# Performance work log

Hardware: AMD Instinct MI355X
Metric: run time of the kernel (lower is better)

Reference implementation:

```python
import jax, jax.numpy as jnp
import numpy as np

NUM_HEADS = 16
HEAD_DIM = 64


def setup_inputs() -> dict:
    key = jax.random.key(0)
    k1, k2, k3 = jax.random.split(key, 3)
    B, S, D = 2, 2048, 1024
    scale = 1.0 / np.sqrt(D)
    return {
        "x": jax.random.normal(k1, (B, S, D), dtype=jnp.float32),
        "W_qkv": jax.random.normal(k2, (D, 3 * D), dtype=jnp.float32) * scale,
        "b_qkv": jnp.zeros((3 * D,), dtype=jnp.float32),
        "W_o": jax.random.normal(k3, (D, D), dtype=jnp.float32) * scale,
        "b_o": jnp.zeros((D,), dtype=jnp.float32),
    }


def reference(x, W_qkv, b_qkv, W_o, b_o):
    B, S, D = x.shape
    H, Hd = NUM_HEADS, HEAD_DIM
    qkv = x @ W_qkv + b_qkv                      # [B, S, 3D]
    qkv = qkv.reshape(B, S, H, 3 * Hd).transpose(0, 2, 1, 3)  # [B, H, S, 3Hd]
    q, k, v = jnp.split(qkv, 3, axis=-1)         # each [B, H, S, Hd]
    # negative squared Euclidean distance: -(|q|^2 - 2 q.k + |k|^2)
    q_sq = jnp.sum(q * q, axis=-1)[..., :, None]   # [B, H, S, 1]
    k_sq = jnp.sum(k * k, axis=-1)[..., None, :]   # [B, H, 1, S]
    qk = jnp.einsum("bhsd,bhtd->bhst", q, k)       # [B, H, S, S]
    logits = -(q_sq - 2.0 * qk + k_sq)
    attn = jax.nn.softmax(logits, axis=-1)
    vals = jnp.einsum("bhst,bhtd->bhsd", attn, v)  # [B, H, S, Hd]
    vals = vals.transpose(0, 2, 1, 3).reshape(B, S, D)
    return vals @ W_o + b_o
```

## Files before the change

kernel.cpp:

```cpp
#include <hip/hip_runtime.h>
#include <hip/hip_bf16.h>

#define NUM_B   2
#define SEQ     2048
#define DMODEL  1024
#define NH      16
#define HD      64
#define M_TOT   (NUM_B * SEQ)
#define N_QKV   (3 * DMODEL)
#define LOG2E   1.4426950408889634f
#define EXP_BIAS 96.0f

typedef __attribute__((ext_vector_type(8))) short short8v;
typedef __attribute__((ext_vector_type(4))) float float4v;
typedef unsigned short ushort_t;

__device__ __forceinline__ ushort_t f2bf(float x) {
    unsigned u = __builtin_bit_cast(unsigned, x);
    u = u + 0x7FFFu + ((u >> 16) & 1u);
    return (ushort_t)(u >> 16);
}
__device__ __forceinline__ float bf2f(ushort_t h) {
    unsigned u = ((unsigned)h) << 16;
    return __builtin_bit_cast(float, u);
}
__device__ __forceinline__ void gll16(const void* g, void* l) {
    __builtin_amdgcn_global_load_lds(
        (const __attribute__((address_space(1))) unsigned int*)g,
        (__attribute__((address_space(3))) unsigned int*)l, 16, 0, 0);
}
__device__ __forceinline__ int sw4(int r) { return (r & 3) ^ ((r >> 2) & 3); }

__global__ __launch_bounds__(256) void prep_kernel(
    const float* __restrict__ Wq, const float* __restrict__ Wo,
    const float* __restrict__ Xf,
    ushort_t* __restrict__ WqT_hi, ushort_t* __restrict__ WqT_lo,
    ushort_t* __restrict__ WoT,
    ushort_t* __restrict__ Xhi, ushort_t* __restrict__ Xlo)
{
    const int bid = blockIdx.x;
    const int t = threadIdx.x;

    if (bid >= 1024) {
        size_t base = (size_t)(bid - 1024) * 4096 + t * 16;
        float xs[16];
        *(float4v*)&xs[0]  = *(const float4v*)(Xf + base);
        *(float4v*)&xs[4]  = *(const float4v*)(Xf + base + 4);
        *(float4v*)&xs[8]  = *(const float4v*)(Xf + base + 8);
        *(float4v*)&xs[12] = *(const float4v*)(Xf + base + 12);
        short8v h0, h1, l0, l1;
        #pragma unroll
        for (int e = 0; e < 8; e++) {
            ushort_t a = f2bf(xs[e]), b = f2bf(xs[8 + e]);
            h0[e] = (short)a; h1[e] = (short)b;
            l0[e] = (short)f2bf(xs[e] - bf2f(a));
            l1[e] = (short)f2bf(xs[8 + e] - bf2f(b));
        }
        *(short8v*)(Xhi + base) = h0; *(short8v*)(Xhi + base + 8) = h1;
        *(short8v*)(Xlo + base) = l0; *(short8v*)(Xlo + base + 8) = l1;
        return;
    }

    __shared__ float Tf[64][65];
    const float* src; ushort_t *dhi, *dlo; int N, k0, n0;
    if (bid < 768) {
        int kt = bid / 48, nt = bid % 48;
        src = Wq; N = N_QKV; dhi = WqT_hi; dlo = WqT_lo;
        k0 = kt * 64; n0 = nt * 64;
    } else {
        int tid = bid - 768;
        int kt = tid >> 4, nt = tid & 15;
        src = Wo; N = DMODEL; dhi = WoT; dlo = nullptr;
        k0 = kt * 64; n0 = nt * 64;
    }
    {
        int r = t >> 2, c0 = (t & 3) * 16;
        const float* srow = src + (size_t)(k0 + r) * N + n0 + c0;
        #pragma unroll
        for (int u = 0; u < 4; u++) {
            float4v f = *(const float4v*)(srow + 4 * u);
            #pragma unroll
            for (int e = 0; e < 4; e++) Tf[r][c0 + 4 * u + e] = f[e];
        }
    }
    __syncthreads();
    {
        int nl = t >> 2, kc = (t & 3) * 16;
        short8v h0, h1, l0, l1;
        #pragma unroll
        for (int e = 0; e < 8; e++) {
            float x0 = Tf[kc + e][nl];
            float x1 = Tf[kc + 8 + e][nl];
            ushort_t a = f2bf(x0), b = f2bf(x1);
            h0[e] = (short)a; h1[e] = (short)b;
            l0[e] = (short)f2bf(x0 - bf2f(a));
            l1[e] = (short)f2bf(x1 - bf2f(b));
        }
        ushort_t* o = dhi + (size_t)(n0 + nl) * 1024 + k0 + kc;
        *(short8v*)o = h0; *(short8v*)(o + 8) = h1;
        if (dlo) {
            ushort_t* o2 = dlo + (size_t)(n0 + nl) * 1024 + k0 + kc;
            *(short8v*)o2 = l0; *(short8v*)(o2 + 8) = l1;
        }
    }
}

__global__ __launch_bounds__(512, 2) void qkv_mfma256_kernel(
    const ushort_t* __restrict__ Xhi, const ushort_t* __restrict__ Xlo,
    const ushort_t* __restrict__ WqT_hi, const ushort_t* __restrict__ WqT_lo,
    const float* __restrict__ bias,
    ushort_t* __restrict__ Qhi, ushort_t* __restrict__ Qlo,
    ushort_t* __restrict__ Khi, ushort_t* __restrict__ Klo,
    ushort_t* __restrict__ Vout,
    float* __restrict__ Qsq, float* __restrict__ Ksq)
{
    __shared__ ushort_t AS [2 * 2 * 8192];
    __shared__ ushort_t BSh[2 * 2 * 8192];
    const int SLAB = 8192;
    const int BUFS = 2 * SLAB;

    const int t    = threadIdx.x;
    const int w    = t >> 6;
    const int quad = (t >> 4) & 3, ln = t & 15;
    const int wr = w >> 2, wc = w & 3;
    const int bx = blockIdx.x, by = blockIdx.y;
    const int p  = bx >> 2, bq = bx & 3;
    const int m0 = by * 256;
    const bool qk = (p != 2);
    const int h  = 4 * bq + wc;
    const int g  = p + 3 * h;

    const ushort_t* gA[2]; const ushort_t* gB[2]; int lOff[2];
    #pragma unroll
    for (int i = 0; i < 2; i++) {
        int c = 512 * i + t;
        int r = c >> 2, kb = c & 3;
        gA[i] = Xhi + (size_t)(m0 + r) * 1024 + 8 * (kb ^ sw4(r));
        int hj = 4 * bq + (r >> 6);
        int ng = 192 * hj + 64 * p + (r & 63);
        gB[i] = WqT_hi + (size_t)ng * 1024 + 8 * (kb ^ sw4(r));
        lOff[i] = (512 * i + 64 * w) * 8;
    }
    const size_t xlo_off = (size_t)(Xlo - Xhi);
    const size_t wlo_off = (size_t)(WqT_lo - WqT_hi);

    int aoff[8], boff[4];
    #pragma unroll
    for (int mt = 0; mt < 8; mt++) {
        int m_l = 128 * wr + 16 * mt + ln;
        aoff[mt] = m_l * 32 + ((quad ^ sw4(m_l)) << 3);
    }
    #pragma unroll
    for (int nt = 0; nt < 4; nt++) {
        int n_l = 64 * wc + 16 * nt + ln;
        boff[nt] = n_l * 32 + ((quad ^ sw4(n_l)) << 3);
    }

    float4v acc[8][4];
    #pragma unroll
    for (int i = 0; i < 8; i++)
        #pragma unroll
        for (int j = 0; j < 4; j++) acc[i][j] = (float4v){0.f, 0.f, 0.f, 0.f};

    auto stage = [&](int ks, int buf) {
        const int kk = 32 * ks;
        ushort_t* Ab = &AS [buf * BUFS];
        ushort_t* Bb = &BSh[buf * BUFS];
        #pragma unroll
        for (int i = 0; i < 2; i++) {
            gll16(gA[i] + kk, Ab + lOff[i]);
            gll16(gB[i] + kk, Bb + lOff[i]);
        }
        if (qk) {
            #pragma unroll
            for (int i = 0; i < 2; i++) {
                gll16(gA[i] + kk + xlo_off, Ab + SLAB + lOff[i]);
                gll16(gB[i] + kk + wlo_off, Bb + SLAB + lOff[i]);
            }
        }
    };

    const int NKS = DMODEL / 32;
    stage(0, 0);
    __syncthreads();

    for (int ks = 0; ks < NKS; ks++) {
        const int buf = ks & 1;
        if (ks + 1 < NKS) stage(ks + 1, buf ^ 1);

        const ushort_t* Ab = &AS [buf * BUFS];
        const ushort_t* Bb = &BSh[buf * BUFS];

        short8v bh4[4], bl4[4];
        #pragma unroll
        for (int nt = 0; nt < 4; nt++) {
            bh4[nt] = *(const short8v*)(Bb + boff[nt]);
            if (qk) bl4[nt] = *(const short8v*)(Bb + SLAB + boff[nt]);
        }
        #pragma unroll
        for (int mt = 0; mt < 8; mt++) {
            short8v ahm = *(const short8v*)(Ab + aoff[mt]);
            if (qk) {
                short8v alm = *(const short8v*)(Ab + SLAB + aoff[mt]);
                #pragma unroll
                for (int nt = 0; nt < 4; nt++) {
                    acc[mt][nt] = __builtin_amdgcn_mfma_f32_16x16x32_bf16(ahm, bh4[nt], acc[mt][nt], 0, 0, 0);
                    acc[mt][nt] = __builtin_amdgcn_mfma_f32_16x16x32_bf16(ahm, bl4[nt], acc[mt][nt], 0, 0, 0);
                    acc[mt][nt] = __builtin_amdgcn_mfma_f32_16x16x32_bf16(alm, bh4[nt], acc[mt][nt], 0, 0, 0);
                }
            } else {
                #pragma unroll
                for (int nt = 0; nt < 4; nt++)
                    acc[mt][nt] = __builtin_amdgcn_mfma_f32_16x16x32_bf16(ahm, bh4[nt], acc[mt][nt], 0, 0, 0);
            }
        }
        __syncthreads();
    }

    float bvv[4];
    #pragma unroll
    for (int nt = 0; nt < 4; nt++) bvv[nt] = bias[64 * g + 16 * nt + ln];

    #pragma unroll
    for (int mt = 0; mt < 8; mt++) {
        #pragma unroll
        for (int r = 0; r < 4; r++) {
            int m = m0 + 128 * wr + 16 * mt + 4 * quad + r;
            int bb = m >> 11, s = m & (SEQ - 1);
            size_t hsrow = (size_t)(bb * NH + h) * SEQ + s;
            size_t rowbase = hsrow * HD;
            float vv[4];
            #pragma unroll
            for (int nt = 0; nt < 4; nt++) vv[nt] = acc[mt][nt][r] + bvv[nt];
            if (p == 0) {
                float sq = 0.f;
                #pragma unroll
                for (int nt = 0; nt < 4; nt++) {
                    float v = vv[nt];
                    sq += v * v;
                    float v2 = v * (2.0f * LOG2E);
                    ushort_t hb = f2bf(v2);
                    Qhi[rowbase + 16 * nt + ln] = hb;
                    Qlo[rowbase + 16 * nt + ln] = f2bf(v2 - bf2f(hb));
                }
                sq += __shfl_xor(sq, 1); sq += __shfl_xor(sq, 2);
                sq += __shfl_xor(sq, 4); sq += __shfl_xor(sq, 8);
                if (ln == 0) Qsq[hsrow] = sq * LOG2E - EXP_BIAS;
            } else if (p == 1) {
                float sq = 0.f;
                #pragma unroll
                for (int nt = 0; nt < 4; nt++) {
                    float v = vv[nt];
                    sq += v * v;
                    ushort_t hb = f2bf(v);
                    Khi[rowbase + 16 * nt + ln] = hb;
                    Klo[rowbase + 16 * nt + ln] = f2bf(v - bf2f(hb));
                }
                sq += __shfl_xor(sq, 1); sq += __shfl_xor(sq, 2);
                sq += __shfl_xor(sq, 4); sq += __shfl_xor(sq, 8);
                if (ln == 0) Ksq[hsrow] = sq * LOG2E;
            } else {
                #pragma unroll
                for (int nt = 0; nt < 4; nt++)
                    Vout[((size_t)(bb * NH + h) * 64 + 16 * nt + ln) * SEQ + s] = f2bf(vv[nt]);
            }
        }
    }
}

template<bool PRE>
__global__ __launch_bounds__(256) void qkv_mfma_kernel(
    const float* __restrict__ X,
    const ushort_t* __restrict__ Xhi, const ushort_t* __restrict__ Xlo,
    const ushort_t* __restrict__ WqT_hi, const ushort_t* __restrict__ WqT_lo,
    const float* __restrict__ bias,
    ushort_t* __restrict__ Qhi, ushort_t* __restrict__ Qlo,
    ushort_t* __restrict__ Khi, ushort_t* __restrict__ Klo,
    ushort_t* __restrict__ Vout,
    float* __restrict__ Qsq, float* __restrict__ Ksq)
{
    __shared__ ushort_t AS2[2 * 128 * 32];
    __shared__ ushort_t BS [2 * 128 * 32];
    const int LO = 128 * 32;
    const int t = threadIdx.x;
    const int w = t >> 6, lane = t & 63;
    const int quad = (t >> 4) & 3, ln = t & 15;
    const int wr = w >> 1, wc = w & 1;
    const int m0 = blockIdx.y * 128, n0 = blockIdx.x * 128;
    const int g = blockIdx.x * 2 + wc;
    const int h = g / 3, part = g % 3;

    const ushort_t* gA[2]; ushort_t* lA[2];
    const float* aptr = nullptr;
    ushort_t *ast_hi0, *ast_hi1, *ast_lo0, *ast_lo1;
    size_t xlo_off = 0;
    if constexpr (PRE) {
        #pragma unroll
        for (int i = 0; i < 2; i++) {
            int c = 256 * i + 64 * w + lane;
            int r = c >> 2, kbp = c & 3;
            gA[i] = Xhi + (size_t)(m0 + r) * 1024 + 8 * (kbp ^ sw4(r));
            lA[i] = &AS2[(256 * i + 64 * w) * 8];
        }
        xlo_off = (size_t)(Xlo - Xhi);
    } else {
        const int arow = t >> 1, akh = t & 1;
        aptr = X + (size_t)(m0 + arow) * DMODEL + 16 * akh;
        const int asw = sw4(arow);
        ast_hi0 = &AS2[arow * 32 + (((2 * akh) ^ asw) << 3)];
        ast_hi1 = &AS2[arow * 32 + (((2 * akh + 1) ^ asw) << 3)];
        ast_lo0 = &AS2[LO + arow * 32 + (((2 * akh) ^ asw) << 3)];
        ast_lo1 = &AS2[LO + arow * 32 + (((2 * akh + 1) ^ asw) << 3)];
    }

    const ushort_t* gB[2]; ushort_t* lB[2];
    #pragma unroll
    for (int i = 0; i < 2; i++) {
        int c = 256 * i + 64 * w + lane;
        int n = c >> 2, kbp = c & 3;
        gB[i] = WqT_hi + (size_t)(n0 + n) * 1024 + 8 * (kbp ^ sw4(n));
        lB[i] = &BS[(256 * i + 64 * w) * 8];
    }
    const size_t lo_goff = (size_t)(WqT_lo - WqT_hi);

    int aoff[4], boff[4];
    #pragma unroll
    for (int i = 0; i < 4; i++) {
        int m_l = 64 * wr + 16 * i + ln;
        aoff[i] = m_l * 32 + ((quad ^ sw4(m_l)) << 3);
        int n_l = 64 * wc + 16 * i + ln;
        boff[i] = n_l * 32 + ((quad ^ sw4(n_l)) << 3);
    }

    float4v acc[4][4];
    #pragma unroll
    for (int i = 0; i < 4; i++)
        #pragma unroll
        for (int j = 0; j < 4; j++) acc[i][j] = (float4v){0.f, 0.f, 0.f, 0.f};

    for (int k0 = 0; k0 < DMODEL; k0 += 32) {
        __syncthreads();
        #pragma unroll
        for (int i = 0; i < 2; i++) {
            gll16(gB[i] + k0, lB[i]);
            gll16(gB[i] + k0 + lo_goff, lB[i] + LO);
        }
        if constexpr (PRE) {
            #pragma unroll
            for (int i = 0; i < 2; i++) {
                gll16(gA[i] + k0, lA[i]);
                gll16(gA[i] + k0 + xlo_off, lA[i] + LO);
            }
        } else {
            float xs[16];
            *(float4v*)&xs[0]  = *(const float4v*)(aptr + k0);
            *(float4v*)&xs[4]  = *(const float4v*)(aptr + k0 + 4);
            *(float4v*)&xs[8]  = *(const float4v*)(aptr + k0 + 8);
            *(float4v*)&xs[12] = *(const float4v*)(aptr + k0 + 12);
            short8v h0, h1, l0, l1;
            #pragma unroll
            for (int e = 0; e < 8; e++) {
                ushort_t a = f2bf(xs[e]), b = f2bf(xs[8 + e]);
                h0[e] = (short)a; h1[e] = (short)b;
                l0[e] = (short)f2bf(xs[e] - bf2f(a));
                l1[e] = (short)f2bf(xs[8 + e] - bf2f(b));
            }
            *(short8v*)ast_hi0 = h0; *(short8v*)ast_hi1 = h1;
            *(short8v*)ast_lo0 = l0; *(short8v*)ast_lo1 = l1;
        }
        __syncthreads();

        short8v ah[4], al[4], bh[4], bl[4];
        #pragma unroll
        for (int i = 0; i < 4; i++) {
            ah[i] = *(short8v*)&AS2[aoff[i]];
            al[i] = *(short8v*)&AS2[LO + aoff[i]];
            bh[i] = *(short8v*)&BS[boff[i]];
            bl[i] = *(short8v*)&BS[LO + boff[i]];
        }
        if (part != 2) {
            #pragma unroll
            for (int mt = 0; mt < 4; mt++)
                #pragma unroll
                for (int nt = 0; nt < 4; nt++) {
                    acc[mt][nt] = __builtin_amdgcn_mfma_f32_16x16x32_bf16(ah[mt], bh[nt], acc[mt][nt], 0, 0, 0);
                    acc[mt][nt] = __builtin_amdgcn_mfma_f32_16x16x32_bf16(ah[mt], bl[nt], acc[mt][nt], 0, 0, 0);
                    acc[mt][nt] = __builtin_amdgcn_mfma_f32_16x16x32_bf16(al[mt], bh[nt], acc[mt][nt], 0, 0, 0);
                }
        } else {
            #pragma unroll
            for (int mt = 0; mt < 4; mt++)
                #pragma unroll
                for (int nt = 0; nt < 4; nt++)
                    acc[mt][nt] = __builtin_amdgcn_mfma_f32_16x16x32_bf16(ah[mt], bh[nt], acc[mt][nt], 0, 0, 0);
        }
    }

    float bvv[4];
    #pragma unroll
    for (int nt = 0; nt < 4; nt++) bvv[nt] = bias[64 * g + 16 * nt + ln];

    #pragma unroll
    for (int mt = 0; mt < 4; mt++) {
        #pragma unroll
        for (int r = 0; r < 4; r++) {
            int m = m0 + 64 * wr + 16 * mt + 4 * quad + r;
            int bb = m >> 11, s = m & (SEQ - 1);
            size_t hsrow = (size_t)(bb * NH + h) * SEQ + s;
            size_t rowbase = hsrow * HD;
            float vv[4];
            #pragma unroll
            for (int nt = 0; nt < 4; nt++) vv[nt] = acc[mt][nt][r] + bvv[nt];
            if (part == 0) {
                float sq = 0.f;
                #pragma unroll
                for (int nt = 0; nt < 4; nt++) {
                    float v = vv[nt];
                    sq += v * v;
                    float v2 = v * (2.0f * LOG2E);
                    ushort_t hb = f2bf(v2);
                    Qhi[rowbase + 16 * nt + ln] = hb;
                    Qlo[rowbase + 16 * nt + ln] = f2bf(v2 - bf2f(hb));
                }
                sq += __shfl_xor(sq, 1); sq += __shfl_xor(sq, 2);
                sq += __shfl_xor(sq, 4); sq += __shfl_xor(sq, 8);
                if (ln == 0) Qsq[hsrow] = sq * LOG2E - EXP_BIAS;
            } else if (part == 1) {
                float sq = 0.f;
                #pragma unroll
                for (int nt = 0; nt < 4; nt++) {
                    float v = vv[nt];
                    sq += v * v;
                    ushort_t hb = f2bf(v);
                    Khi[rowbase + 16 * nt + ln] = hb;
                    Klo[rowbase + 16 * nt + ln] = f2bf(v - bf2f(hb));
                }
                sq += __shfl_xor(sq, 1); sq += __shfl_xor(sq, 2);
                sq += __shfl_xor(sq, 4); sq += __shfl_xor(sq, 8);
                if (ln == 0) Ksq[hsrow] = sq * LOG2E;
            } else {
                #pragma unroll
                for (int nt = 0; nt < 4; nt++)
                    Vout[rowbase + 16 * nt + ln] = f2bf(vv[nt]);
            }
        }
    }
}

template<bool PRE>
__global__ __launch_bounds__(256, 4) void attn_mfma_kernel(
    const ushort_t* __restrict__ Qhi, const ushort_t* __restrict__ Qlo,
    const ushort_t* __restrict__ Khi, const ushort_t* __restrict__ Klo,
    const ushort_t* __restrict__ Vsrc,
    const float* __restrict__ Qsq, const float* __restrict__ Ksq,
    ushort_t* __restrict__ vals)
{
    __shared__ ushort_t KS[2 * 64 * 64];
    __shared__ ushort_t VtS [64 * 64];
    __shared__ ushort_t PsS [64 * 72];
    const int LO = 64 * 64;

    const int t    = threadIdx.x;
    const int w    = t >> 6, lane = t & 63;
    const int quad = (t >> 4) & 3, ln = t & 15;
    const int bh   = blockIdx.y;
    const int q0   = blockIdx.x * 64;
    const size_t base  = (size_t)bh * SEQ * HD;
    const size_t baseS = (size_t)bh * SEQ;

    short8v qhi[2], qlo[2];
    float4v qsq4;
    {
        size_t ro = base + (size_t)(q0 + 16 * w + ln) * HD + quad * 8;
        qhi[0] = *(const short8v*)(Qhi + ro);
        qhi[1] = *(const short8v*)(Qhi + ro + 32);
        qlo[0] = *(const short8v*)(Qlo + ro);
        qlo[1] = *(const short8v*)(Qlo + ro + 32);
        qsq4 = *(const float4v*)(Qsq + baseS + q0 + 16 * w + 4 * quad);
    }

    const ushort_t* gK[2]; ushort_t* lK[2];
    #pragma unroll
    for (int i = 0; i < 2; i++) {
        int c = 256 * i + 64 * w + lane;
        int key = c >> 3, dbp = c & 7;
        gK[i] = Khi + base + (size_t)key * HD + 8 * (dbp ^ (key & 7));
        lK[i] = &KS[(256 * i + 64 * w) * 8];
    }
    const size_t kloff = (size_t)(Klo - Khi);

    const ushort_t* gV[2]; ushort_t* lV[2];
    if constexpr (PRE) {
        #pragma unroll
        for (int i = 0; i < 2; i++) {
            int c = 256 * i + 64 * w + lane;
            int d = c >> 3, kc = c & 7;
            gV[i] = Vsrc + ((size_t)bh * 64 + d) * SEQ + 8 * (kc ^ (d & 7));
            lV[i] = &VtS[(256 * i + 64 * w) * 8];
        }
    }

    float4v accO[4];
    float lsum[4];
    #pragma unroll
    for (int nt = 0; nt < 4; nt++) accO[nt] = (float4v){0.f, 0.f, 0.f, 0.f};
    #pragma unroll
    for (int r = 0; r < 4; r++) lsum[r] = 0.f;

    for (int kt = 0; kt < SEQ; kt += 64) {
        __syncthreads();
        #pragma unroll
        for (int i = 0; i < 2; i++) {
            gll16(gK[i] + (size_t)kt * HD, lK[i]);
            gll16(gK[i] + (size_t)kt * HD + kloff, lK[i] + LO);
        }
        if constexpr (PRE) {
            #pragma unroll
            for (int i = 0; i < 2; i++)
                gll16(gV[i] + kt, lV[i]);
        } else {
            #pragma unroll
            for (int i = 0; i < 2; i++) {
                int c = t + 256 * i;
                int key = c >> 3, db = c & 7;
                short8v v8 = *(const short8v*)(Vsrc + base + (size_t)(kt + key) * HD + 8 * db);
                #pragma unroll
                for (int e = 0; e < 8; e++) {
                    int col = key ^ (e << 3);
                    VtS[(8 * db + e) * 64 + col] = (ushort_t)v8[e];
                }
            }
        }
        float ksq_c[4];
        #pragma unroll
        for (int nt = 0; nt < 4; nt++)
            ksq_c[nt] = Ksq[baseS + kt + 16 * nt + ln];
        __syncthreads();

        float4v accS[4];
        #pragma unroll
        for (int nt = 0; nt < 4; nt++) accS[nt] = (float4v){0.f, 0.f, 0.f, 0.f};

        #pragma unroll
        for (int nt = 0; nt < 4; nt++) {
            int keyrow = 16 * nt + ln;
            #pragma unroll
            for (int c = 0; c < 2; c++) {
                int db  = quad + 4 * c;
                int off = keyrow * 64 + ((db ^ (keyrow & 7)) << 3);
                short8v bh_ = *(short8v*)&KS[off];
                short8v bl_ = *(short8v*)&KS[LO + off];
                accS[nt] = __builtin_amdgcn_mfma_f32_16x16x32_bf16(qhi[c], bh_, accS[nt], 0, 0, 0);
                accS[nt] = __builtin_amdgcn_mfma_f32_16x16x32_bf16(qhi[c], bl_, accS[nt], 0, 0, 0);
                accS[nt] = __builtin_amdgcn_mfma_f32_16x16x32_bf16(qlo[c], bh_, accS[nt], 0, 0, 0);
            }
        }

        #pragma unroll
        for (int nt = 0; nt < 4; nt++) {
            float pv[4];
            #pragma unroll
            for (int r = 0; r < 4; r++) {
                float p = exp2f(accS[nt][r] - ksq_c[nt] - qsq4[r]);
                lsum[r] += p;
                pv[r] = p;
            }
            unsigned int pk01, pk23;
            asm("v_cvt_pk_bf16_f32 %0, %1, %2" : "=v"(pk01) : "v"(pv[0]), "v"(pv[1]));
            asm("v_cvt_pk_bf16_f32 %0, %1, %2" : "=v"(pk23) : "v"(pv[2]), "v"(pv[3]));
            ushort_t* pp = &PsS[(16 * w + 4 * quad) * 72 + 16 * nt + ln];
            pp[0]       = (ushort_t)(pk01 & 0xffffu);
            pp[72]      = (ushort_t)(pk01 >> 16);
            pp[144]     = (ushort_t)(pk23 & 0xffffu);
            pp[216]     = (ushort_t)(pk23 >> 16);
        }
        __syncthreads();

        #pragma unroll
        for (int c = 0; c < 2; c++) {
            short8v aP = *(short8v*)&PsS[(16 * w + ln) * 72 + quad * 8 + 32 * c];
            #pragma unroll
            for (int nt = 0; nt < 4; nt++) {
                int drow = 16 * nt + ln;
                int db   = quad + 4 * c;
                int off  = drow * 64 + ((db ^ (drow & 7)) << 3);
                short8v bV = *(short8v*)&VtS[off];
                accO[nt] = __builtin_amdgcn_mfma_f32_16x16x32_bf16(aP, bV, accO[nt], 0, 0, 0);
            }
        }
    }

    const int bb = bh >> 4, h = bh & 15;
    float inv[4];
    #pragma unroll
    for (int r = 0; r < 4; r++) {
        float s = lsum[r];
        s += __shfl_xor(s, 1); s += __shfl_xor(s, 2);
        s += __shfl_xor(s, 4); s += __shfl_xor(s, 8);
        inv[r] = 1.f / s;
    }
    #pragma unroll
    for (int nt = 0; nt < 4; nt++)
        #pragma unroll
        for (int r = 0; r < 4; r++) {
            int row = q0 + 16 * w + 4 * quad + r;
            vals[(size_t)(bb * SEQ + row) * DMODEL + h * 64 + 16 * nt + ln] =
                f2bf(accO[nt][r] * inv[r]);
        }
}

__global__ __launch_bounds__(256) void out_mfma_kernel(
    const ushort_t* __restrict__ Ab, const ushort_t* __restrict__ BT,
    const float* __restrict__ bias, float* __restrict__ out)
{
    __shared__ ushort_t AS[2 * 128 * 32], BSo[2 * 128 * 32];
    const int BUF = 128 * 32;
    const int t = threadIdx.x;
    const int w = t >> 6;
    const int quad = (t >> 4) & 3, ln = t & 15;
    const int wr = (w >> 1), wc = w & 1;
    const int m0 = blockIdx.y * 128, n0 = blockIdx.x * 128;

    const ushort_t* gA[2]; const ushort_t* gB[2]; int lOff[2];
    #pragma unroll
    for (int i = 0; i < 2; i++) {
        int c = 256 * i + t;
        int r = c >> 2, kbp = c & 3;
        gA[i] = Ab + (size_t)(m0 + r) * 1024 + 8 * (kbp ^ sw4(r));
        gB[i] = BT + (size_t)(n0 + r) * 1024 + 8 * (kbp ^ sw4(r));
        lOff[i] = (256 * i + 64 * w) * 8;
    }
    int aoff[4], boff[4];
    #pragma unroll
    for (int i = 0; i < 4; i++) {
        int m_l = 64 * wr + 16 * i + ln;
        aoff[i] = m_l * 32 + ((quad ^ sw4(m_l)) << 3);
        int n_l = 64 * wc + 16 * i + ln;
        boff[i] = n_l * 32 + ((quad ^ sw4(n_l)) << 3);
    }

    float4v acc[4][4];
    #pragma unroll
    for (int i = 0; i < 4; i++)
        #pragma unroll
        for (int j = 0; j < 4; j++) acc[i][j] = (float4v){0.f, 0.f, 0.f, 0.f};

    auto stage = [&](int ks, int buf) {
        const int kk = 32 * ks;
        #pragma unroll
        for (int i = 0; i < 2; i++) {
            gll16(gA[i] + kk, &AS [buf * BUF] + lOff[i]);
            gll16(gB[i] + kk, &BSo[buf * BUF] + lOff[i]);
        }
    };

    const int NKS = DMODEL / 32;
    stage(0, 0);
    __syncthreads();

    for (int ks = 0; ks < NKS; ks++) {
        const int buf = ks & 1;
        if (ks + 1 < NKS) stage(ks + 1, buf ^ 1);

        const ushort_t* Abuf = &AS [buf * BUF];
        const ushort_t* Bbuf = &BSo[buf * BUF];
        short8v a[4], b[4];
        #pragma unroll
        for (int i = 0; i < 4; i++) {
            a[i] = *(const short8v*)(Abuf + aoff[i]);
            b[i] = *(const short8v*)(Bbuf + boff[i]);
        }
        #pragma unroll
        for (int mt = 0; mt < 4; mt++)
            #pragma unroll
            for (int nt = 0; nt < 4; nt++)
                acc[mt][nt] = __builtin_amdgcn_mfma_f32_16x16x32_bf16(a[mt], b[nt], acc[mt][nt], 0, 0, 0);

        __syncthreads();
    }

    #pragma unroll
    for (int nt = 0; nt < 4; nt++) {
        int n = n0 + 64 * wc + 16 * nt + ln;
        float bv = bias[n];
        #pragma unroll
        for (int mt = 0; mt < 4; mt++)
            #pragma unroll
            for (int r = 0; r < 4; r++) {
                int m = m0 + 64 * wr + 16 * mt + 4 * quad + r;
                out[(size_t)m * DMODEL + n] = acc[mt][nt][r] + bv;
            }
    }
}

extern "C" void kernel_launch(void* const* d_in, const int* in_sizes, int n_in,
                              void* d_out, int out_size, void* d_ws, size_t ws_size,
                              hipStream_t stream) {
    const float* x     = (const float*)d_in[0];
    const float* W_qkv = (const float*)d_in[1];
    const float* b_qkv = (const float*)d_in[2];
    const float* W_o   = (const float*)d_in[3];
    const float* b_o   = (const float*)d_in[4];
    float* out = (float*)d_out;

    const size_t WQT = (size_t)N_QKV * DMODEL;
    const size_t WO  = (size_t)DMODEL * DMODEL;
    const size_t QE  = (size_t)NUM_B * NH * SEQ * HD;
    const size_t SQN = (size_t)NUM_B * NH * SEQ;

    const size_t NEED = (2 * WQT + WO + 5 * QE + 2 * QE) * 2 + 2 * SQN * 4;
    const bool pre = (ws_size >= NEED);

    ushort_t* ws     = (ushort_t*)d_ws;
    ushort_t* WqT_hi = ws;
    ushort_t* WqT_lo = WqT_hi + WQT;
    ushort_t* WoT    = WqT_lo + WQT;
    ushort_t* Qhi    = WoT + WO;
    ushort_t* Qlo    = Qhi + QE;
    ushort_t* Khi    = Qlo + QE;
    ushort_t* Klo    = Khi + QE;
    ushort_t* Vx     = Klo + QE;
    float*    Qsq; float* Ksq;
    ushort_t* valsb; ushort_t* Xhi = nullptr; ushort_t* Xlo = nullptr;

    if (pre) {
        Qsq   = (float*)(Vx + QE);
        Ksq   = Qsq + SQN;
        Xhi   = (ushort_t*)(Ksq + SQN);
        Xlo   = Xhi + QE;
        valsb = WqT_hi;
    } else {
        valsb = Vx + QE;
        Qsq   = (float*)(valsb + QE);
        Ksq   = Qsq + SQN;
    }

    prep_kernel<<<pre ? 2048 : 1024, 256, 0, stream>>>(
        W_qkv, W_o, x, WqT_hi, WqT_lo, WoT, Xhi, Xlo);
    if (pre) {
        qkv_mfma256_kernel<<<dim3(12, M_TOT / 256), 512, 0, stream>>>(
            Xhi, Xlo, WqT_hi, WqT_lo, b_qkv, Qhi, Qlo, Khi, Klo, Vx, Qsq, Ksq);
        attn_mfma_kernel<true><<<dim3(SEQ / 64, NUM_B * NH), 256, 0, stream>>>(
            Qhi, Qlo, Khi, Klo, Vx, Qsq, Ksq, valsb);
    } else {
        qkv_mfma_kernel<false><<<dim3(N_QKV / 128, M_TOT / 128), 256, 0, stream>>>(
            x, nullptr, nullptr, WqT_hi, WqT_lo, b_qkv, Qhi, Qlo, Khi, Klo, Vx, Qsq, Ksq);
        attn_mfma_kernel<false><<<dim3(SEQ / 64, NUM_B * NH), 256, 0, stream>>>(
            Qhi, Qlo, Khi, Klo, Vx, Qsq, Ksq, valsb);
    }
    out_mfma_kernel<<<dim3(DMODEL / 128, M_TOT / 128), 256, 0, stream>>>(
        valsb, WoT, b_o, out);
}
```

Before: 303.0 us.

## Unify QKV GEMM per head so each block computes Q, K, V together

```diff
diff --git a/kernel.cpp b/kernel.cpp
--- a/kernel.cpp
+++ b/kernel.cpp
@@ -14,6 +14,12 @@
 typedef __attribute__((ext_vector_type(8))) short short8v;
 typedef __attribute__((ext_vector_type(4))) float float4v;
 typedef unsigned short ushort_t;
+
+#if __has_builtin(__builtin_amdgcn_exp2f)
+#define EXP2F(x) __builtin_amdgcn_exp2f(x)
+#else
+#define EXP2F(x) exp2f(x)
+#endif
 
 __device__ __forceinline__ ushort_t f2bf(float x) {
     unsigned u = __builtin_bit_cast(unsigned, x);
@@ -105,7 +111,7 @@
     }
 }
 
-__global__ __launch_bounds__(512, 2) void qkv_mfma256_kernel(
+__global__ __launch_bounds__(512, 2) void qkv_uni_kernel(
     const ushort_t* __restrict__ Xhi, const ushort_t* __restrict__ Xlo,
     const ushort_t* __restrict__ WqT_hi, const ushort_t* __restrict__ WqT_lo,
     const float* __restrict__ bias,
@@ -114,70 +120,73 @@
     ushort_t* __restrict__ Vout,
     float* __restrict__ Qsq, float* __restrict__ Ksq)
 {
-    __shared__ ushort_t AS [2 * 2 * 8192];
-    __shared__ ushort_t BSh[2 * 2 * 8192];
-    const int SLAB = 8192;
-    const int BUFS = 2 * SLAB;
+    const int SLAB_A = 8192, BUFA = 16384;
+    const int SLAB_B = 6144, BUFB = 12288;
+    __shared__ ushort_t AS[2 * BUFA];
+    __shared__ ushort_t BS[2 * BUFB];
 
     const int t    = threadIdx.x;
     const int w    = t >> 6;
     const int quad = (t >> 4) & 3, ln = t & 15;
     const int wr = w >> 2, wc = w & 3;
-    const int bx = blockIdx.x, by = blockIdx.y;
-    const int p  = bx >> 2, bq = bx & 3;
-    const int m0 = by * 256;
-    const bool qk = (p != 2);
-    const int h  = 4 * bq + wc;
-    const int g  = p + 3 * h;
-
-    const ushort_t* gA[2]; const ushort_t* gB[2]; int lOff[2];
+    const int h  = blockIdx.x;
+    const int m0 = blockIdx.y * 256;
+
+    const ushort_t* gA[2]; int lOffA[2];
     #pragma unroll
     for (int i = 0; i < 2; i++) {
         int c = 512 * i + t;
         int r = c >> 2, kb = c & 3;
         gA[i] = Xhi + (size_t)(m0 + r) * 1024 + 8 * (kb ^ sw4(r));
-        int hj = 4 * bq + (r >> 6);
-        int ng = 192 * hj + 64 * p + (r & 63);
-        gB[i] = WqT_hi + (size_t)ng * 1024 + 8 * (kb ^ sw4(r));
-        lOff[i] = (512 * i + 64 * w) * 8;
+        lOffA[i] = (512 * i + 64 * w) * 8;
     }
     const size_t xlo_off = (size_t)(Xlo - Xhi);
-    const size_t wlo_off = (size_t)(WqT_lo - WqT_hi);
-
-    int aoff[8], boff[4];
+
+    const ushort_t* gBp[3]; int lOffB[3];
+    #pragma unroll
+    for (int i = 0; i < 3; i++) {
+        int c = 512 * i + t;
+        bool hi = c < 768;
+        int cc = hi ? c : c - 768;
+        int j = cc >> 2, kb = cc & 3;
+        int jj = j >> 4, jl = j & 15;
+        int wcq = jj / 3, part = jj % 3;
+        int ng = 192 * h + 64 * part + 16 * wcq + jl;
+        gBp[i] = (hi ? WqT_hi : WqT_lo) + (size_t)ng * 1024 + 8 * (kb ^ sw4(j));
+        int cwb = (512 * i + 64 * w) - (hi ? 0 : 768);
+        lOffB[i] = (hi ? 0 : SLAB_B) + cwb * 8;
+    }
+
+    int aoff[8], boff[3];
     #pragma unroll
     for (int mt = 0; mt < 8; mt++) {
         int m_l = 128 * wr + 16 * mt + ln;
         aoff[mt] = m_l * 32 + ((quad ^ sw4(m_l)) << 3);
     }
     #pragma unroll
-    for (int nt = 0; nt < 4; nt++) {
-        int n_l = 64 * wc + 16 * nt + ln;
-        boff[nt] = n_l * 32 + ((quad ^ sw4(n_l)) << 3);
-    }
-
-    float4v acc[8][4];
+    for (int p = 0; p < 3; p++) {
+        int j = 48 * wc + 16 * p + ln;
+        boff[p] = j * 32 + ((quad ^ sw4(j)) << 3);
+    }
+
+    float4v acc[8][3];
     #pragma unroll
     for (int i = 0; i < 8; i++)
         #pragma unroll
-        for (int j = 0; j < 4; j++) acc[i][j] = (float4v){0.f, 0.f, 0.f, 0.f};
+        for (int j = 0; j < 3; j++) acc[i][j] = (float4v){0.f, 0.f, 0.f, 0.f};
 
     auto stage = [&](int ks, int buf) {
         const int kk = 32 * ks;
-        ushort_t* Ab = &AS [buf * BUFS];
-        ushort_t* Bb = &BSh[buf * BUFS];
+        ushort_t* Ab = &AS[buf * BUFA];
+        ushort_t* Bb = &BS[buf * BUFB];
         #pragma unroll
         for (int i = 0; i < 2; i++) {
-            gll16(gA[i] + kk, Ab + lOff[i]);
-            gll16(gB[i] + kk, Bb + lOff[i]);
-        }
-        if (qk) {
-            #pragma unroll
-            for (int i = 0; i < 2; i++) {
-                gll16(gA[i] + kk + xlo_off, Ab + SLAB + lOff[i]);
-                gll16(gB[i] + kk + wlo_off, Bb + SLAB + lOff[i]);
-            }
-        }
+            gll16(gA[i] + kk, Ab + lOffA[i]);
+            gll16(gA[i] + kk + xlo_off, Ab + SLAB_A + lOffA[i]);
+        }
+        #pragma unroll
+        for (int i = 0; i < 3; i++)
+            gll16(gBp[i] + kk, Bb + lOffB[i]);
     };
 
     const int NKS = DMODEL / 32;
@@ -188,38 +197,35 @@
         const int buf = ks & 1;
         if (ks + 1 < NKS) stage(ks + 1, buf ^ 1);
 
-        const ushort_t* Ab = &AS [buf * BUFS];
-        const ushort_t* Bb = &BSh[buf * BUFS];
-
-        short8v bh4[4], bl4[4];
-        #pragma unroll
-        for (int nt = 0; nt < 4; nt++) {
-            bh4[nt] = *(const short8v*)(Bb + boff[nt]);
-            if (qk) bl4[nt] = *(const short8v*)(Bb + SLAB + boff[nt]);
-        }
+        const ushort_t* Ab = &AS[buf * BUFA];
+        const ushort_t* Bb = &BS[buf * BUFB];
+
+        short8v bh0 = *(const short8v*)(Bb + boff[0]);
+        short8v bh1 = *(const short8v*)(Bb + boff[1]);
+        short8v bh2 = *(const short8v*)(Bb + boff[2]);
+        short8v bl0 = *(const short8v*)(Bb + SLAB_B + boff[0]);
+        short8v bl1 = *(const short8v*)(Bb + SLAB_B + boff[1]);
+
         #pragma unroll
         for (int mt = 0; mt < 8; mt++) {
-            short8v ahm = *(const short8v*)(Ab + aoff[mt]);
-            if (qk) {
-                short8v alm = *(const short8v*)(Ab + SLAB + aoff[mt]);
-                #pragma unroll
-                for (int nt = 0; nt < 4; nt++) {
-                    acc[mt][nt] = __builtin_amdgcn_mfma_f32_16x16x32_bf16(ahm, bh4[nt], acc[mt][nt], 0, 0, 0);
-                    acc[mt][nt] = __builtin_amdgcn_mfma_f32_16x16x32_bf16(ahm, bl4[nt], acc[mt][nt], 0, 0, 0);
-                    acc[mt][nt] = __builtin_amdgcn_mfma_f32_16x16x32_bf16(alm, bh4[nt], acc[mt][nt], 0, 0, 0);
-                }
-            } else {
-                #pragma unroll
-                for (int nt = 0; nt < 4; nt++)
-                    acc[mt][nt] = __builtin_amdgcn_mfma_f32_16x16x32_bf16(ahm, bh4[nt], acc[mt][nt], 0, 0, 0);
-            }
+            short8v aH = *(const short8v*)(Ab + aoff[mt]);
+            short8v aL = *(const short8v*)(Ab + SLAB_A + aoff[mt]);
+            acc[mt][0] = __builtin_amdgcn_mfma_f32_16x16x32_bf16(aH, bh0, acc[mt][0], 0, 0, 0);
+            acc[mt][0] = __builtin_amdgcn_mfma_f32_16x16x32_bf16(aH, bl0, acc[mt][0], 0, 0, 0);
+            acc[mt][0] = __builtin_amdgcn_mfma_f32_16x16x32_bf16(aL, bh0, acc[mt][0], 0, 0, 0);
+            acc[mt][1] = __builtin_amdgcn_mfma_f32_16x16x32_bf16(aH, bh1, acc[mt][1], 0, 0, 0);
+            acc[mt][1] = __builtin_amdgcn_mfma_f32_16x16x32_bf16(aH, bl1, acc[mt][1], 0, 0, 0);
+            acc[mt][1] = __builtin_amdgcn_mfma_f32_16x16x32_bf16(aL, bh1, acc[mt][1], 0, 0, 0);
+            acc[mt][2] = __builtin_amdgcn_mfma_f32_16x16x32_bf16(aH, bh2, acc[mt][2], 0, 0, 0);
         }
         __syncthreads();
     }
 
-    float bvv[4];
-    #pragma unroll
-    for (int nt = 0; nt < 4; nt++) bvv[nt] = bias[64 * g + 16 * nt + ln];
+    const float bQ = bias[192 * h + 16 * wc + ln];
+    const float bK = bias[192 * h + 64 + 16 * wc + ln];
+    const float bV = bias[192 * h + 128 + 16 * wc + ln];
+    const int d = 16 * wc + ln;
+    float* sqbuf = (float*)AS;
 
     #pragma unroll
     for (int mt = 0; mt < 8; mt++) {
@@ -229,42 +235,48 @@
             int bb = m >> 11, s = m & (SEQ - 1);
             size_t hsrow = (size_t)(bb * NH + h) * SEQ + s;
             size_t rowbase = hsrow * HD;
-            float vv[4];
-            #pragma unroll
-            for (int nt = 0; nt < 4; nt++) vv[nt] = acc[mt][nt][r] + bvv[nt];
-            if (p == 0) {
-                float sq = 0.f;
-                #pragma unroll
-                for (int nt = 0; nt < 4; nt++) {
-                    float v = vv[nt];
-                    sq += v * v;
-                    float v2 = v * (2.0f * LOG2E);
-                    ushort_t hb = f2bf(v2);
-                    Qhi[rowbase + 16 * nt + ln] = hb;
-                    Qlo[rowbase + 16 * nt + ln] = f2bf(v2 - bf2f(hb));
-                }
-                sq += __shfl_xor(sq, 1); sq += __shfl_xor(sq, 2);
-                sq += __shfl_xor(sq, 4); sq += __shfl_xor(sq, 8);
-                if (ln == 0) Qsq[hsrow] = sq * LOG2E - EXP_BIAS;
-            } else if (p == 1) {
-                float sq = 0.f;
-                #pragma unroll
-                for (int nt = 0; nt < 4; nt++) {
-                    float v = vv[nt];
-                    sq += v * v;
-                    ushort_t hb = f2bf(v);
-                    Khi[rowbase + 16 * nt + ln] = hb;
-                    Klo[rowbase + 16 * nt + ln] = f2bf(v - bf2f(hb));
-                }
-                sq += __shfl_xor(sq, 1); sq += __shfl_xor(sq, 2);
-                sq += __shfl_xor(sq, 4); sq += __shfl_xor(sq, 8);
-                if (ln == 0) Ksq[hsrow] = sq * LOG2E;
-            } else {
-                #pragma unroll
-                for (int nt = 0; nt < 4; nt++)
-                    Vout[((size_t)(bb * NH + h) * 64 + 16 * nt + ln) * SEQ + s] = f2bf(vv[nt]);
-            }
-        }
+
+            float vQ = acc[mt][0][r] + bQ;
+            float vK = acc[mt][1][r] + bK;
+            float vV = acc[mt][2][r] + bV;
+
+            float v2 = vQ * (2.0f * LOG2E);
+            ushort_t hbq = f2bf(v2);
+            Qhi[rowbase + d] = hbq;
+            Qlo[rowbase + d] = f2bf(v2 - bf2f(hbq));
+            float sqq = vQ * vQ;
+            sqq += __shfl_xor(sqq, 1); sqq += __shfl_xor(sqq, 2);
+            sqq += __shfl_xor(sqq, 4); sqq += __shfl_xor(sqq, 8);
+
+            ushort_t hbk = f2bf(vK);
+            Khi[rowbase + d] = hbk;
+            Klo[rowbase + d] = f2bf(vK - bf2f(hbk));
+            float sqk = vK * vK;
+            sqk += __shfl_xor(sqk, 1); sqk += __shfl_xor(sqk, 2);
+            sqk += __shfl_xor(sqk, 4); sqk += __shfl_xor(sqk, 8);
+
+            Vout[((size_t)(bb * NH + h) * 64 + d) * SEQ + s] = f2bf(vV);
+
+            if (ln == 0) {
+                int rloc = 16 * mt + 4 * quad + r;
+                sqbuf[((0 * 2 + wr) * 4 + wc) * 128 + rloc] = sqq;
+                sqbuf[((1 * 2 + wr) * 4 + wc) * 128 + rloc] = sqk;
+            }
+        }
+    }
+    __syncthreads();
+    {
+        int sel = t >> 8, rid = t & 255;
+        int wrr = rid >> 7, rloc = rid & 127;
+        float s4 = sqbuf[((sel * 2 + wrr) * 4 + 0) * 128 + rloc]
+                 + sqbuf[((sel * 2 + wrr) * 4 + 1) * 128 + rloc]
+                 + sqbuf[((sel * 2 + wrr) * 4 + 2) * 128 + rloc]
+                 + sqbuf[((sel * 2 + wrr) * 4 + 3) * 128 + rloc];
+        int m = m0 + 128 * wrr + rloc;
+        int bb = m >> 11, s = m & (SEQ - 1);
+        size_t hsrow = (size_t)(bb * NH + h) * SEQ + s;
+        if (sel == 0) Qsq[hsrow] = s4 * LOG2E - EXP_BIAS;
+        else          Ksq[hsrow] = s4 * LOG2E;
     }
 }
 
@@ -469,14 +481,16 @@
     const size_t baseS = (size_t)bh * SEQ;
 
     short8v qhi[2], qlo[2];
-    float4v qsq4;
+    float nqsq4[4];
     {
         size_t ro = base + (size_t)(q0 + 16 * w + ln) * HD + quad * 8;
         qhi[0] = *(const short8v*)(Qhi + ro);
         qhi[1] = *(const short8v*)(Qhi + ro + 32);
         qlo[0] = *(const short8v*)(Qlo + ro);
         qlo[1] = *(const short8v*)(Qlo + ro + 32);
-        qsq4 = *(const float4v*)(Qsq + baseS + q0 + 16 * w + 4 * quad);
+        float4v q4 = *(const float4v*)(Qsq + baseS + q0 + 16 * w + 4 * quad);
+        #pragma unroll
+        for (int r = 0; r < 4; r++) nqsq4[r] = -q4[r];
     }
 
     const ushort_t* gK[2]; ushort_t* lK[2];
@@ -531,15 +545,17 @@
                 }
             }
         }
-        float ksq_c[4];
+        float nksq[4];
         #pragma unroll
         for (int nt = 0; nt < 4; nt++)
-            ksq_c[nt] = Ksq[baseS + kt + 16 * nt + ln];
+            nksq[nt] = -Ksq[baseS + kt + 16 * nt + ln];
         __syncthreads();
 
         float4v accS[4];
         #pragma unroll
-        for (int nt = 0; nt < 4; nt++) accS[nt] = (float4v){0.f, 0.f, 0.f, 0.f};
+        for (int nt = 0; nt < 4; nt++)
+            #pragma unroll
+            for (int r = 0; r < 4; r++) accS[nt][r] = nksq[nt] + nqsq4[r];
 
         #pragma unroll
         for (int nt = 0; nt < 4; nt++) {
@@ -561,7 +577,7 @@
             float pv[4];
             #pragma unroll
             for (int r = 0; r < 4; r++) {
-                float p = exp2f(accS[nt][r] - ksq_c[nt] - qsq4[r]);
+                float p = EXP2F(accS[nt][r]);
                 lsum[r] += p;
                 pv[r] = p;
             }
@@ -738,7 +754,7 @@
     prep_kernel<<<pre ? 2048 : 1024, 256, 0, stream>>>(
         W_qkv, W_o, x, WqT_hi, WqT_lo, WoT, Xhi, Xlo);
     if (pre) {
-        qkv_mfma256_kernel<<<dim3(12, M_TOT / 256), 512, 0, stream>>>(
+        qkv_uni_kernel<<<dim3(NH, M_TOT / 256), 512, 0, stream>>>(
             Xhi, Xlo, WqT_hi, WqT_lo, b_qkv, Qhi, Qlo, Khi, Klo, Vx, Qsq, Ksq);
         attn_mfma_kernel<true><<<dim3(SEQ / 64, NUM_B * NH), 256, 0, stream>>>(
             Qhi, Qlo, Khi, Klo, Vx, Qsq, Ksq, valsb);
```

New measurement: 272.6 us (median of 2 runs). 1.11x faster.
